# Performance work log

Measured on AMD Instinct MI355X. Metric: run time of the kernel, lower is better.

Reference implementation:

```python
import jax, jax.numpy as jnp
import numpy as np

B = 131072
FLOW_SIZE = 16
PASS = 8
TRANS = FLOW_SIZE - PASS  # 8
N_BINS = 128
HIDDEN = 256


def setup_inputs() -> dict:
    key = jax.random.key(0)
    k0, k1, k2 = jax.random.split(key, 3)
    x = jax.random.uniform(k0, (B, FLOW_SIZE + 1), dtype=jnp.float32)
    W1 = jax.random.normal(k1, (PASS, HIDDEN), dtype=jnp.float32) * 0.3
    b1 = jnp.zeros((HIDDEN,), dtype=jnp.float32)
    W2 = jax.random.normal(k2, (HIDDEN, TRANS * N_BINS), dtype=jnp.float32) * 0.05
    b2 = jnp.zeros((TRANS * N_BINS,), dtype=jnp.float32)
    return {"x": x, "W1": W1, "b1": b1, "W2": W2, "b2": b2}


def reference(x, W1, b1, W2, b2):
    xA = x[:, :PASS]                      # [B, P]
    xB = x[:, PASS:FLOW_SIZE]             # [B, T]
    jacobian = x[:, FLOW_SIZE:FLOW_SIZE + 1]  # [B, 1]

    # NN: small MLP, exp output -> positive unnormalized bin widths Q [B, T, n_bins]
    h = jax.nn.relu(xA @ W1 + b1)
    Q = jnp.exp(h @ W2 + b2).reshape(x.shape[0], TRANS, N_BINS)

    Qsum = jnp.cumsum(Q, axis=-1)                     # [B, T, n_bins]
    Qnorms = Qsum[:, :, -1:]                          # [B, T, 1]
    Q = Q / (Qnorms / N_BINS)                         # normalized slopes
    Qsum = Qsum / Qnorms                              # normalized CDF
    Qsum = jnp.pad(Qsum, ((0, 0), (0, 0), (1, 0)))    # left-pad CDF with 0

    alphas = xB * N_BINS
    bins = jnp.floor(alphas)
    alphas = (alphas - bins) / N_BINS                 # fractional offset within bin
    bins = jnp.clip(bins.astype(jnp.int32), 0, N_BINS - 1)

    cdf_int_part = jnp.take_along_axis(Qsum, bins[..., None], axis=-1)[..., 0]  # [B, T]
    cdf_float_part = jnp.take_along_axis(Q, bins[..., None], axis=-1)[..., 0]   # [B, T]

    cdf = cdf_float_part * alphas + cdf_int_part      # [B, T]
    jacobian = jacobian * jnp.prod(cdf_float_part, axis=-1, keepdims=True)  # [B, 1]

    return jnp.concatenate((xA, cdf, jacobian), axis=-1)  # [B, flow_size+1]
```

## Files before the change

### kernel.cpp

```cpp
#include <hip/hip_runtime.h>
#include <math.h>

#define NROWS 131072
#define XC    17
#define ROWSB 128
#define HID   256
#define NB    128
#define NCOL  1024
#define LOG2E 1.44269504088896340736f

typedef __attribute__((ext_vector_type(8))) short bf16x8;
typedef __attribute__((ext_vector_type(4))) float f32x4;

#if __has_builtin(__builtin_amdgcn_exp2f)
#define EXP2F(v) __builtin_amdgcn_exp2f(v)
#else
#define EXP2F(v) exp2f(v)
#endif
#if __has_builtin(__builtin_amdgcn_rcpf)
#define RCPF(v) __builtin_amdgcn_rcpf(v)
#else
#define RCPF(v) (1.f / (v))
#endif

__device__ __forceinline__ unsigned short f2bf(float f) {
    unsigned int u = __float_as_uint(f);
    return (unsigned short)((u + 0x7FFFu + ((u >> 16) & 1u)) >> 16);
}

__device__ __forceinline__ float red16(float v) {
    int x;
    x = __builtin_amdgcn_update_dpp(0, __float_as_int(v), 0xB1, 0xF, 0xF, true);
    v += __int_as_float(x);
    x = __builtin_amdgcn_update_dpp(0, __float_as_int(v), 0x4E, 0xF, 0xF, true);
    v += __int_as_float(x);
    x = __builtin_amdgcn_update_dpp(0, __float_as_int(v), 0x141, 0xF, 0xF, true);
    v += __int_as_float(x);
    x = __builtin_amdgcn_update_dpp(0, __float_as_int(v), 0x140, 0xF, 0xF, true);
    v += __int_as_float(x);
    return v;
}

__global__ void prep_w2(const float* __restrict__ W2, unsigned short* __restrict__ w2t) {
    __shared__ __align__(16) unsigned short tkT[32][80];
    const int tid = threadIdx.x;
    const int k0 = (blockIdx.x & 3) * 64;
    const int c0 = (blockIdx.x >> 2) * 32;
    const int c4 = (tid & 7) * 4;
    const int kk = (tid >> 3) * 2;
    const float4 r0 = *(const float4*)&W2[(size_t)(k0 + kk) * NCOL + c0 + c4];
    const float4 r1 = *(const float4*)&W2[(size_t)(k0 + kk + 1) * NCOL + c0 + c4];
    const float v0[4] = {r0.x, r0.y, r0.z, r0.w};
    const float v1[4] = {r1.x, r1.y, r1.z, r1.w};
    #pragma unroll
    for (int i = 0; i < 4; ++i) {
        const unsigned int p = (unsigned int)f2bf(v0[i] * LOG2E)
                             | ((unsigned int)f2bf(v1[i] * LOG2E) << 16);
        *(unsigned int*)&tkT[c4 + i][kk] = p;
    }
    __syncthreads();
    const int g = tid & 7, c = tid >> 3;
    const uint4 q = *(const uint4*)&tkT[c][g * 8];
    *(uint4*)&w2t[(size_t)(c0 + c) * HID + k0 + ((g ^ (c & 7)) << 3)] = q;
}

__global__ __launch_bounds__(256, 2)
void gplc6(const float* __restrict__ x,
           const float* __restrict__ W1,
           const float* __restrict__ b1,
           const unsigned short* __restrict__ w2t,
           const float* __restrict__ b2,
           float* __restrict__ out)
{
    __shared__ float xs[ROWSB * XC];
    __shared__ __align__(16) union {
        unsigned short hb[ROWSB * HID];
        struct { unsigned short w2[2][NB * 64]; float b2s[NCOL]; } g;
    } u;

    const int tid  = threadIdx.x;
    const int lane = tid & 63;
    const int w    = tid >> 6;
    const int quad = lane >> 4;
    const int l15  = lane & 15;
    const int wr   = w * 32;
    const int ksw  = (lane & 7) << 3;
    const size_t r0 = (size_t)blockIdx.x * ROWSB;

    for (int i = tid; i < ROWSB * XC; i += 256) xs[i] = x[r0 * XC + i];
    const int cp = tid & 127, hlf = tid >> 7;
    float w1r[16];
    #pragma unroll
    for (int i = 0; i < 8; ++i) {
        const float2 t2 = *(const float2*)&W1[i * HID + 2 * cp];
        w1r[2 * i] = t2.x; w1r[2 * i + 1] = t2.y;
    }
    const float2 b1v = *(const float2*)&b1[2 * cp];
    __syncthreads();

    for (int r = 0; r < 64; ++r) {
        const int row = hlf * 64 + r;
        float a0 = b1v.x, a1 = b1v.y;
        #pragma unroll
        for (int i = 0; i < 8; ++i) {
            const float xv = xs[row * XC + i];
            a0 = fmaf(xv, w1r[2 * i], a0);
            a1 = fmaf(xv, w1r[2 * i + 1], a1);
        }
        a0 = fmaxf(a0, 0.f); a1 = fmaxf(a1, 0.f);
        const int eidx = row * HID + (((cp >> 2) ^ (row & 15)) << 3) + ((cp & 3) << 1);
        *(unsigned int*)&u.hb[eidx] = (unsigned int)f2bf(a0) | ((unsigned int)f2bf(a1) << 16);
    }
    __syncthreads();

    bf16x8 afr[2][8];
    #pragma unroll
    for (int rt = 0; rt < 2; ++rt)
        #pragma unroll
        for (int kf = 0; kf < 8; ++kf) {
            const int row = wr + rt * 16 + l15;
            afr[rt][kf] = *(const bf16x8*)&u.hb[row * HID + (((kf * 4 + quad) ^ l15) << 3)];
        }
    __syncthreads();

    for (int i = tid; i < NCOL; i += 256) u.g.b2s[i] = b2[i] * LOG2E;

    auto stage = [&](int n) {
        const int t = n >> 2, kc = n & 3, buf = n & 1;
        #pragma unroll
        for (int j = 0; j < 4; ++j) {
            const int ob = (w * 4 + j) * 512;
            const int c  = (ob >> 6) + (lane >> 3);
            const int kl = (lane & 7) << 3;
            const unsigned short* gp = w2t + (size_t)(t * NB + c) * HID + kc * 64 + kl;
            unsigned short* lp = &u.g.w2[buf][ob];
            __builtin_amdgcn_global_load_lds(
                (const __attribute__((address_space(1))) unsigned int*)gp,
                (__attribute__((address_space(3))) unsigned int*)lp, 16, 0, 0);
        }
    };

    float jf[2][4] = {{1.f,1.f,1.f,1.f},{1.f,1.f,1.f,1.f}};

    stage(0);
    #pragma unroll 1
    for (int t = 0; t < 8; ++t) {
        f32x4 acc[2][8];
        #pragma unroll
        for (int rt = 0; rt < 2; ++rt)
            #pragma unroll
            for (int ct = 0; ct < 8; ++ct) acc[rt][ct] = (f32x4){0.f, 0.f, 0.f, 0.f};

        #pragma unroll
        for (int kc = 0; kc < 4; ++kc) {
            __syncthreads();
            const int n = t * 4 + kc;
            if (n < 31) stage(n + 1);
            const unsigned short* wsb = u.g.w2[kc & 1];
            #pragma unroll
            for (int ks = 0; ks < 2; ++ks) {
                const int kf = kc * 2 + ks;
                const int klog = ks * 32 + quad * 8;
                #pragma unroll
                for (int ct = 0; ct < 8; ++ct) {
                    const int c = ct * 16 + l15;
                    const bf16x8 bf = *(const bf16x8*)&wsb[c * 64 + (klog ^ ksw)];
                    acc[0][ct] = __builtin_amdgcn_mfma_f32_16x16x32_bf16(afr[0][kf], bf, acc[0][ct], 0, 0, 0);
                    acc[1][ct] = __builtin_amdgcn_mfma_f32_16x16x32_bf16(afr[1][kf], bf, acc[1][ct], 0, 0, 0);
                }
            }
        }

        float bb[8];
        #pragma unroll
        for (int ct = 0; ct < 8; ++ct) bb[ct] = u.g.b2s[t * NB + ct * 16 + l15];
        #pragma unroll
        for (int rt = 0; rt < 2; ++rt)
            #pragma unroll
            for (int i = 0; i < 4; ++i) {
                const int row = wr + rt * 16 + quad * 4 + i;
                const float alpha = xs[row * XC + 8 + t] * 128.f;
                const float fb = floorf(alpha);
                const int bin = min(max((int)fb, 0), 127);
                const float fr = alpha - fb;
                float e[8];
                #pragma unroll
                for (int ct = 0; ct < 8; ++ct) e[ct] = EXP2F(acc[rt][ct][i] + bb[ct]);
                const float P1 = e[0],      P2 = P1 + e[1], P3 = P2 + e[2], P4 = P3 + e[3];
                const float P5 = P4 + e[4], P6 = P5 + e[5], P7 = P6 + e[6], P8 = P7 + e[7];
                int thr = (bin - l15 + 15) >> 4;
                thr = min(max(thr, 0), 8);
                const float sA = (thr & 1) ? P1 : 0.f;
                const float sB = (thr & 1) ? P3 : P2;
                const float sC = (thr & 1) ? P5 : P4;
                const float sD = (thr & 1) ? P7 : P6;
                const float sE = (thr & 2) ? sB : sA;
                const float sF = (thr & 2) ? sD : sC;
                float num = (thr & 4) ? sF : sE;
                num = (thr >= 8) ? P8 : num;
                const int cb = bin >> 4;
                const float t1 = (cb & 1) ? e[1] : e[0];
                const float t2 = (cb & 1) ? e[3] : e[2];
                const float t3 = (cb & 1) ? e[5] : e[4];
                const float t4 = (cb & 1) ? e[7] : e[6];
                const float u1 = (cb & 2) ? t2 : t1;
                const float u2 = (cb & 2) ? t4 : t3;
                const float es = (cb & 4) ? u2 : u1;
                float eb  = ((bin & 15) == l15) ? es : 0.f;
                float tot = P8;
                tot = red16(tot); num = red16(num); eb = red16(eb);
                const float inv = RCPF(tot);
                jf[rt][i] *= 128.f * eb * inv;
                if (l15 == 0) xs[row * XC + 8 + t] = fmaf(eb, fr, num) * inv;
            }
    }

    if (l15 == 0) {
        #pragma unroll
        for (int rt = 0; rt < 2; ++rt)
            #pragma unroll
            for (int i = 0; i < 4; ++i) {
                const int row = wr + rt * 16 + quad * 4 + i;
                xs[row * XC + 16] *= jf[rt][i];
            }
    }
    __syncthreads();
    for (int i = tid; i < ROWSB * XC; i += 256) out[r0 * XC + i] = xs[i];
}

extern "C" void kernel_launch(void* const* d_in, const int* in_sizes, int n_in,
                              void* d_out, int out_size, void* d_ws, size_t ws_size,
                              hipStream_t stream) {
    (void)in_sizes; (void)n_in; (void)ws_size; (void)out_size;
    prep_w2<<<128, 256, 0, stream>>>((const float*)d_in[3], (unsigned short*)d_ws);
    gplc6<<<NROWS / ROWSB, 256, 0, stream>>>(
        (const float*)d_in[0], (const float*)d_in[1], (const float*)d_in[2],
        (const unsigned short*)d_ws, (const float*)d_in[4], (float*)d_out);
}
```

Before: 175.1 us.

## Halve rows per block to raise occupancy and read b2 directly from global

Cuts rows per block from 128 to 64, so each wave handles one 16-row MFMA tile instead of two, and raises launch bounds to 4 blocks per CU. Shared memory and registers per block shrink, and the b2 staging in LDS is dropped in favour of direct global loads added into the accumulators. The aim is more resident waves to hide memory and sync latency. The cost is that every W2 tile is streamed from L2 twice as often per row, with half as much MFMA work per LDS B-fragment load.

```diff
diff --git a/kernel.cpp b/kernel.cpp
--- a/kernel.cpp
+++ b/kernel.cpp
@@ -3,7 +3,7 @@
 
 #define NROWS 131072
 #define XC    17
-#define ROWSB 128
+#define ROWSB 64
 #define HID   256
 #define NB    128
 #define NCOL  1024
@@ -64,7 +64,7 @@
     *(uint4*)&w2t[(size_t)(c0 + c) * HID + k0 + ((g ^ (c & 7)) << 3)] = q;
 }
 
-__global__ __launch_bounds__(256, 2)
+__global__ __launch_bounds__(256, 4)
 void gplc6(const float* __restrict__ x,
            const float* __restrict__ W1,
            const float* __restrict__ b1,
@@ -75,7 +75,7 @@
     __shared__ float xs[ROWSB * XC];
     __shared__ __align__(16) union {
         unsigned short hb[ROWSB * HID];
-        struct { unsigned short w2[2][NB * 64]; float b2s[NCOL]; } g;
+        unsigned short w2[2][NB * 64];
     } u;
 
     const int tid  = threadIdx.x;
@@ -83,7 +83,7 @@
     const int w    = tid >> 6;
     const int quad = lane >> 4;
     const int l15  = lane & 15;
-    const int wr   = w * 32;
+    const int wr   = w * 16;
     const int ksw  = (lane & 7) << 3;
     const size_t r0 = (size_t)blockIdx.x * ROWSB;
 
@@ -98,8 +98,8 @@
     const float2 b1v = *(const float2*)&b1[2 * cp];
     __syncthreads();
 
-    for (int r = 0; r < 64; ++r) {
-        const int row = hlf * 64 + r;
+    for (int r = 0; r < 32; ++r) {
+        const int row = hlf * 32 + r;
         float a0 = b1v.x, a1 = b1v.y;
         #pragma unroll
         for (int i = 0; i < 8; ++i) {
@@ -113,17 +113,13 @@
     }
     __syncthreads();
 
-    bf16x8 afr[2][8];
+    bf16x8 afr[8];
     #pragma unroll
-    for (int rt = 0; rt < 2; ++rt)
-        #pragma unroll
-        for (int kf = 0; kf < 8; ++kf) {
-            const int row = wr + rt * 16 + l15;
-            afr[rt][kf] = *(const bf16x8*)&u.hb[row * HID + (((kf * 4 + quad) ^ l15) << 3)];
-        }
-    __syncthreads();
-
-    for (int i = tid; i < NCOL; i += 256) u.g.b2s[i] = b2[i] * LOG2E;
+    for (int kf = 0; kf < 8; ++kf) {
+        const int row = wr + l15;
+        afr[kf] = *(const bf16x8*)&u.hb[row * HID + (((kf * 4 + quad) ^ l15) << 3)];
+    }
+    __syncthreads();
 
     auto stage = [&](int n) {
         const int t = n >> 2, kc = n & 3, buf = n & 1;
@@ -133,30 +129,28 @@
             const int c  = (ob >> 6) + (lane >> 3);
             const int kl = (lane & 7) << 3;
             const unsigned short* gp = w2t + (size_t)(t * NB + c) * HID + kc * 64 + kl;
-            unsigned short* lp = &u.g.w2[buf][ob];
+            unsigned short* lp = &u.w2[buf][ob];
             __builtin_amdgcn_global_load_lds(
                 (const __attribute__((address_space(1))) unsigned int*)gp,
                 (__attribute__((address_space(3))) unsigned int*)lp, 16, 0, 0);
         }
     };
 
-    float jf[2][4] = {{1.f,1.f,1.f,1.f},{1.f,1.f,1.f,1.f}};
+    float jf[4] = {1.f, 1.f, 1.f, 1.f};
 
     stage(0);
     #pragma unroll 1
     for (int t = 0; t < 8; ++t) {
-        f32x4 acc[2][8];
-        #pragma unroll
-        for (int rt = 0; rt < 2; ++rt)
-            #pragma unroll
-            for (int ct = 0; ct < 8; ++ct) acc[rt][ct] = (f32x4){0.f, 0.f, 0.f, 0.f};
+        f32x4 acc[8];
+        #pragma unroll
+        for (int ct = 0; ct < 8; ++ct) acc[ct] = (f32x4){0.f, 0.f, 0.f, 0.f};
 
         #pragma unroll
         for (int kc = 0; kc < 4; ++kc) {
             __syncthreads();
             const int n = t * 4 + kc;
             if (n < 31) stage(n + 1);
-            const unsigned short* wsb = u.g.w2[kc & 1];
+            const unsigned short* wsb = u.w2[kc & 1];
             #pragma unroll
             for (int ks = 0; ks < 2; ++ks) {
                 const int kf = kc * 2 + ks;
@@ -165,64 +159,62 @@
                 for (int ct = 0; ct < 8; ++ct) {
                     const int c = ct * 16 + l15;
                     const bf16x8 bf = *(const bf16x8*)&wsb[c * 64 + (klog ^ ksw)];
-                    acc[0][ct] = __builtin_amdgcn_mfma_f32_16x16x32_bf16(afr[0][kf], bf, acc[0][ct], 0, 0, 0);
-                    acc[1][ct] = __builtin_amdgcn_mfma_f32_16x16x32_bf16(afr[1][kf], bf, acc[1][ct], 0, 0, 0);
+                    acc[ct] = __builtin_amdgcn_mfma_f32_16x16x32_bf16(afr[kf], bf, acc[ct], 0, 0, 0);
                 }
             }
         }
 
-        float bb[8];
-        #pragma unroll
-        for (int ct = 0; ct < 8; ++ct) bb[ct] = u.g.b2s[t * NB + ct * 16 + l15];
-        #pragma unroll
-        for (int rt = 0; rt < 2; ++rt)
+        #pragma unroll
+        for (int ct = 0; ct < 8; ++ct) {
+            const float bbv = b2[t * NB + ct * 16 + l15] * LOG2E;
+            acc[ct][0] += bbv; acc[ct][1] += bbv; acc[ct][2] += bbv; acc[ct][3] += bbv;
+        }
+
+        #pragma unroll
+        for (int i = 0; i < 4; ++i) {
+            const int row = wr + quad * 4 + i;
+            const float alpha = xs[row * XC + 8 + t] * 128.f;
+            const float fb = floorf(alpha);
+            const int bin = min(max((int)fb, 0), 127);
+            const float fr = alpha - fb;
+            float e[8];
             #pragma unroll
-            for (int i = 0; i < 4; ++i) {
-                const int row = wr + rt * 16 + quad * 4 + i;
-                const float alpha = xs[row * XC + 8 + t] * 128.f;
-                const float fb = floorf(alpha);
-                const int bin = min(max((int)fb, 0), 127);
-                const float fr = alpha - fb;
-                float e[8];
-                #pragma unroll
-                for (int ct = 0; ct < 8; ++ct) e[ct] = EXP2F(acc[rt][ct][i] + bb[ct]);
-                const float P1 = e[0],      P2 = P1 + e[1], P3 = P2 + e[2], P4 = P3 + e[3];
-                const float P5 = P4 + e[4], P6 = P5 + e[5], P7 = P6 + e[6], P8 = P7 + e[7];
-                int thr = (bin - l15 + 15) >> 4;
-                thr = min(max(thr, 0), 8);
-                const float sA = (thr & 1) ? P1 : 0.f;
-                const float sB = (thr & 1) ? P3 : P2;
-                const float sC = (thr & 1) ? P5 : P4;
-                const float sD = (thr & 1) ? P7 : P6;
-                const float sE = (thr & 2) ? sB : sA;
-                const float sF = (thr & 2) ? sD : sC;
-                float num = (thr & 4) ? sF : sE;
-                num = (thr >= 8) ? P8 : num;
-                const int cb = bin >> 4;
-                const float t1 = (cb & 1) ? e[1] : e[0];
-                const float t2 = (cb & 1) ? e[3] : e[2];
-                const float t3 = (cb & 1) ? e[5] : e[4];
-                const float t4 = (cb & 1) ? e[7] : e[6];
-                const float u1 = (cb & 2) ? t2 : t1;
-                const float u2 = (cb & 2) ? t4 : t3;
-                const float es = (cb & 4) ? u2 : u1;
-                float eb  = ((bin & 15) == l15) ? es : 0.f;
-                float tot = P8;
-                tot = red16(tot); num = red16(num); eb = red16(eb);
-                const float inv = RCPF(tot);
-                jf[rt][i] *= 128.f * eb * inv;
-                if (l15 == 0) xs[row * XC + 8 + t] = fmaf(eb, fr, num) * inv;
-            }
+            for (int ct = 0; ct < 8; ++ct) e[ct] = EXP2F(acc[ct][i]);
+            const float P1 = e[0],      P2 = P1 + e[1], P3 = P2 + e[2], P4 = P3 + e[3];
+            const float P5 = P4 + e[4], P6 = P5 + e[5], P7 = P6 + e[6], P8 = P7 + e[7];
+            int thr = (bin - l15 + 15) >> 4;
+            thr = min(max(thr, 0), 8);
+            const float sA = (thr & 1) ? P1 : 0.f;
+            const float sB = (thr & 1) ? P3 : P2;
+            const float sC = (thr & 1) ? P5 : P4;
+            const float sD = (thr & 1) ? P7 : P6;
+            const float sE = (thr & 2) ? sB : sA;
+            const float sF = (thr & 2) ? sD : sC;
+            float num = (thr & 4) ? sF : sE;
+            num = (thr >= 8) ? P8 : num;
+            const int cb = bin >> 4;
+            const float t1 = (cb & 1) ? e[1] : e[0];
+            const float t2 = (cb & 1) ? e[3] : e[2];
+            const float t3 = (cb & 1) ? e[5] : e[4];
+            const float t4 = (cb & 1) ? e[7] : e[6];
+            const float u1 = (cb & 2) ? t2 : t1;
+            const float u2 = (cb & 2) ? t4 : t3;
+            const float es = (cb & 4) ? u2 : u1;
+            float eb  = ((bin & 15) == l15) ? es : 0.f;
+            float tot = P8;
+            tot = red16(tot); num = red16(num); eb = red16(eb);
+            const float inv = RCPF(tot);
+            jf[i] *= 128.f * eb * inv;
+            if (l15 == 0) xs[row * XC + 8 + t] = fmaf(eb, fr, num) * inv;
+        }
     }
 
     if (l15 == 0) {
         #pragma unroll
-        for (int rt = 0; rt < 2; ++rt)
-            #pragma unroll
-            for (int i = 0; i < 4; ++i) {
-                const int row = wr + rt * 16 + quad * 4 + i;
-                xs[row * XC + 16] *= jf[rt][i];
-            }
+        for (int i = 0; i < 4; ++i) {
+            const int row = wr + quad * 4 + i;
+            xs[row * XC + 16] *= jf[i];
+        }
     }
     __syncthreads();
     for (int i = tid; i < ROWSB * XC; i += 256) out[r0 * XC + i] = xs[i];
```

After: 164.0 us. 6.3% less time.

## Halve rows per block and split waves across row and column halves

Applied to the files above, without the earlier changes.

Each block now handles 64 rows instead of 128. Its four waves form a 2x2 grid over row halves and bin-column halves, and the per-row bin sums, CDF numerator and selected bin are merged across the two column waves through a small LDS buffer. The first-layer MLP reads x directly from global, and the b2 bias is read from global per tile instead of being staged in LDS. The launch bound is raised to three blocks per SM. The aim is more resident blocks and smaller register and LDS use per block. The costs are twice as many blocks each streaming the full W2, and an extra barrier plus merge step per transform dimension.

```diff
diff --git a/kernel.cpp b/kernel.cpp
--- a/kernel.cpp
+++ b/kernel.cpp
@@ -3,7 +3,7 @@
 
 #define NROWS 131072
 #define XC    17
-#define ROWSB 128
+#define ROWSB 64
 #define HID   256
 #define NB    128
 #define NCOL  1024
@@ -64,7 +64,7 @@
     *(uint4*)&w2t[(size_t)(c0 + c) * HID + k0 + ((g ^ (c & 7)) << 3)] = q;
 }
 
-__global__ __launch_bounds__(256, 2)
+__global__ __launch_bounds__(256, 3)
 void gplc6(const float* __restrict__ x,
            const float* __restrict__ W1,
            const float* __restrict__ b1,
@@ -75,15 +75,19 @@
     __shared__ float xs[ROWSB * XC];
     __shared__ __align__(16) union {
         unsigned short hb[ROWSB * HID];
-        struct { unsigned short w2[2][NB * 64]; float b2s[NCOL]; } g;
+        struct {
+            unsigned short w2[2][NB * 64];
+            float mrg[2][ROWSB][4];
+        } g;
     } u;
 
     const int tid  = threadIdx.x;
     const int lane = tid & 63;
     const int w    = tid >> 6;
+    const int rw   = w & 1;
+    const int cw   = w >> 1;
     const int quad = lane >> 4;
     const int l15  = lane & 15;
-    const int wr   = w * 32;
     const int ksw  = (lane & 7) << 3;
     const size_t r0 = (size_t)blockIdx.x * ROWSB;
 
@@ -96,14 +100,14 @@
         w1r[2 * i] = t2.x; w1r[2 * i + 1] = t2.y;
     }
     const float2 b1v = *(const float2*)&b1[2 * cp];
-    __syncthreads();
-
-    for (int r = 0; r < 64; ++r) {
-        const int row = hlf * 64 + r;
+
+    for (int r = 0; r < 32; ++r) {
+        const int row = __builtin_amdgcn_readfirstlane(hlf * 32 + r);
+        const float* xr = x + (r0 + row) * XC;
         float a0 = b1v.x, a1 = b1v.y;
         #pragma unroll
         for (int i = 0; i < 8; ++i) {
-            const float xv = xs[row * XC + i];
+            const float xv = xr[i];
             a0 = fmaf(xv, w1r[2 * i], a0);
             a1 = fmaf(xv, w1r[2 * i + 1], a1);
         }
@@ -118,12 +122,10 @@
     for (int rt = 0; rt < 2; ++rt)
         #pragma unroll
         for (int kf = 0; kf < 8; ++kf) {
-            const int row = wr + rt * 16 + l15;
+            const int row = rw * 32 + rt * 16 + l15;
             afr[rt][kf] = *(const bf16x8*)&u.hb[row * HID + (((kf * 4 + quad) ^ l15) << 3)];
         }
     __syncthreads();
-
-    for (int i = tid; i < NCOL; i += 256) u.g.b2s[i] = b2[i] * LOG2E;
 
     auto stage = [&](int n) {
         const int t = n >> 2, kc = n & 3, buf = n & 1;
@@ -145,11 +147,11 @@
     stage(0);
     #pragma unroll 1
     for (int t = 0; t < 8; ++t) {
-        f32x4 acc[2][8];
+        f32x4 acc[2][4];
         #pragma unroll
         for (int rt = 0; rt < 2; ++rt)
             #pragma unroll
-            for (int ct = 0; ct < 8; ++ct) acc[rt][ct] = (f32x4){0.f, 0.f, 0.f, 0.f};
+            for (int ct = 0; ct < 4; ++ct) acc[rt][ct] = (f32x4){0.f, 0.f, 0.f, 0.f};
 
         #pragma unroll
         for (int kc = 0; kc < 4; ++kc) {
@@ -162,8 +164,8 @@
                 const int kf = kc * 2 + ks;
                 const int klog = ks * 32 + quad * 8;
                 #pragma unroll
-                for (int ct = 0; ct < 8; ++ct) {
-                    const int c = ct * 16 + l15;
+                for (int ct = 0; ct < 4; ++ct) {
+                    const int c = cw * 64 + ct * 16 + l15;
                     const bf16x8 bf = *(const bf16x8*)&wsb[c * 64 + (klog ^ ksw)];
                     acc[0][ct] = __builtin_amdgcn_mfma_f32_16x16x32_bf16(afr[0][kf], bf, acc[0][ct], 0, 0, 0);
                     acc[1][ct] = __builtin_amdgcn_mfma_f32_16x16x32_bf16(afr[1][kf], bf, acc[1][ct], 0, 0, 0);
@@ -171,56 +173,72 @@
             }
         }
 
-        float bb[8];
-        #pragma unroll
-        for (int ct = 0; ct < 8; ++ct) bb[ct] = u.g.b2s[t * NB + ct * 16 + l15];
+        float bb[4];
+        #pragma unroll
+        for (int ct = 0; ct < 4; ++ct)
+            bb[ct] = b2[t * NB + cw * 64 + ct * 16 + l15] * LOG2E;
+
         #pragma unroll
         for (int rt = 0; rt < 2; ++rt)
             #pragma unroll
             for (int i = 0; i < 4; ++i) {
-                const int row = wr + rt * 16 + quad * 4 + i;
+                const int row = rw * 32 + rt * 16 + quad * 4 + i;
                 const float alpha = xs[row * XC + 8 + t] * 128.f;
                 const float fb = floorf(alpha);
                 const int bin = min(max((int)fb, 0), 127);
-                const float fr = alpha - fb;
-                float e[8];
+                float e[4];
                 #pragma unroll
-                for (int ct = 0; ct < 8; ++ct) e[ct] = EXP2F(acc[rt][ct][i] + bb[ct]);
-                const float P1 = e[0],      P2 = P1 + e[1], P3 = P2 + e[2], P4 = P3 + e[3];
-                const float P5 = P4 + e[4], P6 = P5 + e[5], P7 = P6 + e[6], P8 = P7 + e[7];
-                int thr = (bin - l15 + 15) >> 4;
-                thr = min(max(thr, 0), 8);
+                for (int ct = 0; ct < 4; ++ct) e[ct] = EXP2F(acc[rt][ct][i] + bb[ct]);
+                const float P1 = e[0], P2 = P1 + e[1], P3 = P2 + e[2], P4 = P3 + e[3];
+                const int bl = bin - cw * 64;
+                int thr = (bl - l15 + 15) >> 4;
+                thr = min(max(thr, 0), 4);
                 const float sA = (thr & 1) ? P1 : 0.f;
                 const float sB = (thr & 1) ? P3 : P2;
-                const float sC = (thr & 1) ? P5 : P4;
-                const float sD = (thr & 1) ? P7 : P6;
-                const float sE = (thr & 2) ? sB : sA;
-                const float sF = (thr & 2) ? sD : sC;
-                float num = (thr & 4) ? sF : sE;
-                num = (thr >= 8) ? P8 : num;
-                const int cb = bin >> 4;
-                const float t1 = (cb & 1) ? e[1] : e[0];
-                const float t2 = (cb & 1) ? e[3] : e[2];
-                const float t3 = (cb & 1) ? e[5] : e[4];
-                const float t4 = (cb & 1) ? e[7] : e[6];
-                const float u1 = (cb & 2) ? t2 : t1;
-                const float u2 = (cb & 2) ? t4 : t3;
-                const float es = (cb & 4) ? u2 : u1;
-                float eb  = ((bin & 15) == l15) ? es : 0.f;
-                float tot = P8;
+                float num = (thr & 2) ? sB : sA;
+                num = (thr >= 4) ? P4 : num;
+                const int cbl = bl >> 4;
+                const float t1 = (cbl & 1) ? e[1] : e[0];
+                const float t2 = (cbl & 1) ? e[3] : e[2];
+                const float es = (cbl & 2) ? t2 : t1;
+                float eb = (((unsigned)bl < 64u) && ((bin & 15) == l15)) ? es : 0.f;
+                float tot = P4;
                 tot = red16(tot); num = red16(num); eb = red16(eb);
-                const float inv = RCPF(tot);
-                jf[rt][i] *= 128.f * eb * inv;
-                if (l15 == 0) xs[row * XC + 8 + t] = fmaf(eb, fr, num) * inv;
+                if (l15 == 0) {
+                    const f32x4 tr = {tot, num, eb, 0.f};
+                    *(f32x4*)&u.g.mrg[cw][row][0] = tr;
+                }
             }
-    }
-
-    if (l15 == 0) {
+        __syncthreads();
+
+        if (cw == 0) {
+            #pragma unroll
+            for (int rt = 0; rt < 2; ++rt)
+                #pragma unroll
+                for (int i = 0; i < 4; ++i) {
+                    const int row = rw * 32 + rt * 16 + quad * 4 + i;
+                    if (l15 == 0) {
+                        const f32x4 pa = *(const f32x4*)&u.g.mrg[0][row][0];
+                        const f32x4 pb = *(const f32x4*)&u.g.mrg[1][row][0];
+                        const float T   = pa[0] + pb[0];
+                        const float nm  = pa[1] + pb[1];
+                        const float ebv = pa[2] + pb[2];
+                        const float alpha = xs[row * XC + 8 + t] * 128.f;
+                        const float fr = alpha - floorf(alpha);
+                        const float inv = RCPF(T);
+                        jf[rt][i] *= 128.f * ebv * inv;
+                        xs[row * XC + 8 + t] = fmaf(ebv, fr, nm) * inv;
+                    }
+                }
+        }
+    }
+
+    if (cw == 0 && l15 == 0) {
         #pragma unroll
         for (int rt = 0; rt < 2; ++rt)
             #pragma unroll
             for (int i = 0; i < 4; ++i) {
-                const int row = wr + rt * 16 + quad * 4 + i;
+                const int row = rw * 32 + rt * 16 + quad * 4 + i;
                 xs[row * XC + 16] *= jf[rt][i];
             }
     }
```

New measurement: 205.8 us. 1.18x slower.

## Load W2 MFMA fragments directly from global into registers, dropping LDS staging

Applied to the files above, without the earlier changes.

The prep kernel now lays W2 out in MFMA B-fragment order, so each lane loads its bf16x8 operands with coalesced 16-byte global loads straight into registers. These loads are double-buffered across k-slices. This removes the LDS double-buffer, the async global-to-LDS copies, and the per-stage __syncthreads barriers from the GEMM loop. MFMA bursts are wrapped in s_setprio, and b2 is read directly from global. In exchange, every wave re-reads W2 from L2/global instead of sharing one LDS copy per block, and register pressure rises from the two 8-fragment buffers.

```diff
diff --git a/kernel.cpp b/kernel.cpp
--- a/kernel.cpp
+++ b/kernel.cpp
@@ -41,42 +41,35 @@
     return v;
 }
 
-__global__ void prep_w2(const float* __restrict__ W2, unsigned short* __restrict__ w2t) {
-    __shared__ __align__(16) unsigned short tkT[32][80];
-    const int tid = threadIdx.x;
-    const int k0 = (blockIdx.x & 3) * 64;
-    const int c0 = (blockIdx.x >> 2) * 32;
-    const int c4 = (tid & 7) * 4;
-    const int kk = (tid >> 3) * 2;
-    const float4 r0 = *(const float4*)&W2[(size_t)(k0 + kk) * NCOL + c0 + c4];
-    const float4 r1 = *(const float4*)&W2[(size_t)(k0 + kk + 1) * NCOL + c0 + c4];
-    const float v0[4] = {r0.x, r0.y, r0.z, r0.w};
-    const float v1[4] = {r1.x, r1.y, r1.z, r1.w};
+__global__ void prep_w2f(const float* __restrict__ W2, unsigned short* __restrict__ w2f) {
+    const int tid  = threadIdx.x;
+    const int F    = blockIdx.x * 4 + (tid >> 6);
+    const int lane = tid & 63;
+    const int quad = lane >> 4, l15 = lane & 15;
+    const int ct = F & 7, ks = (F >> 3) & 1, kc = (F >> 4) & 3, t = F >> 6;
+    const int k0  = kc * 64 + ks * 32 + quad * 8;
+    const int col = t * NB + ct * 16 + l15;
+    unsigned int p[4];
     #pragma unroll
-    for (int i = 0; i < 4; ++i) {
-        const unsigned int p = (unsigned int)f2bf(v0[i] * LOG2E)
-                             | ((unsigned int)f2bf(v1[i] * LOG2E) << 16);
-        *(unsigned int*)&tkT[c4 + i][kk] = p;
-    }
-    __syncthreads();
-    const int g = tid & 7, c = tid >> 3;
-    const uint4 q = *(const uint4*)&tkT[c][g * 8];
-    *(uint4*)&w2t[(size_t)(c0 + c) * HID + k0 + ((g ^ (c & 7)) << 3)] = q;
+    for (int jj = 0; jj < 4; ++jj) {
+        const unsigned short lo = f2bf(W2[(size_t)(k0 + 2 * jj)     * NCOL + col] * LOG2E);
+        const unsigned short hi = f2bf(W2[(size_t)(k0 + 2 * jj + 1) * NCOL + col] * LOG2E);
+        p[jj] = (unsigned int)lo | ((unsigned int)hi << 16);
+    }
+    uint4 q; q.x = p[0]; q.y = p[1]; q.z = p[2]; q.w = p[3];
+    *(uint4*)&w2f[(size_t)F * 512 + lane * 8] = q;
 }
 
 __global__ __launch_bounds__(256, 2)
 void gplc6(const float* __restrict__ x,
            const float* __restrict__ W1,
            const float* __restrict__ b1,
-           const unsigned short* __restrict__ w2t,
+           const unsigned short* __restrict__ w2f,
            const float* __restrict__ b2,
            float* __restrict__ out)
 {
     __shared__ float xs[ROWSB * XC];
-    __shared__ __align__(16) union {
-        unsigned short hb[ROWSB * HID];
-        struct { unsigned short w2[2][NB * 64]; float b2s[NCOL]; } g;
-    } u;
+    __shared__ __align__(16) unsigned short hb[ROWSB * HID];
 
     const int tid  = threadIdx.x;
     const int lane = tid & 63;
@@ -84,7 +77,6 @@
     const int quad = lane >> 4;
     const int l15  = lane & 15;
     const int wr   = w * 32;
-    const int ksw  = (lane & 7) << 3;
     const size_t r0 = (size_t)blockIdx.x * ROWSB;
 
     for (int i = tid; i < ROWSB * XC; i += 256) xs[i] = x[r0 * XC + i];
@@ -109,7 +101,7 @@
         }
         a0 = fmaxf(a0, 0.f); a1 = fmaxf(a1, 0.f);
         const int eidx = row * HID + (((cp >> 2) ^ (row & 15)) << 3) + ((cp & 3) << 1);
-        *(unsigned int*)&u.hb[eidx] = (unsigned int)f2bf(a0) | ((unsigned int)f2bf(a1) << 16);
+        *(unsigned int*)&hb[eidx] = (unsigned int)f2bf(a0) | ((unsigned int)f2bf(a1) << 16);
     }
     __syncthreads();
 
@@ -119,30 +111,34 @@
         #pragma unroll
         for (int kf = 0; kf < 8; ++kf) {
             const int row = wr + rt * 16 + l15;
-            afr[rt][kf] = *(const bf16x8*)&u.hb[row * HID + (((kf * 4 + quad) ^ l15) << 3)];
+            afr[rt][kf] = *(const bf16x8*)&hb[row * HID + (((kf * 4 + quad) ^ l15) << 3)];
         }
-    __syncthreads();
-
-    for (int i = tid; i < NCOL; i += 256) u.g.b2s[i] = b2[i] * LOG2E;
-
-    auto stage = [&](int n) {
-        const int t = n >> 2, kc = n & 3, buf = n & 1;
-        #pragma unroll
-        for (int j = 0; j < 4; ++j) {
-            const int ob = (w * 4 + j) * 512;
-            const int c  = (ob >> 6) + (lane >> 3);
-            const int kl = (lane & 7) << 3;
-            const unsigned short* gp = w2t + (size_t)(t * NB + c) * HID + kc * 64 + kl;
-            unsigned short* lp = &u.g.w2[buf][ob];
-            __builtin_amdgcn_global_load_lds(
-                (const __attribute__((address_space(1))) unsigned int*)gp,
-                (__attribute__((address_space(3))) unsigned int*)lp, 16, 0, 0);
-        }
+
+    const int loff = lane * 8;
+    auto loadslice = [&](bf16x8* d, int g) {
+        const unsigned short* fp = w2f + (size_t)g * 4096 + loff;
+        #pragma unroll
+        for (int ct = 0; ct < 8; ++ct)
+            d[ct] = *(const bf16x8*)&fp[ct * 512];
     };
 
     float jf[2][4] = {{1.f,1.f,1.f,1.f},{1.f,1.f,1.f,1.f}};
-
-    stage(0);
+    bf16x8 bA[8], bB[8];
+
+#define SLICE_MFMA(CUR, KF)                                                     \
+    {                                                                           \
+        __builtin_amdgcn_s_setprio(1);                                          \
+        _Pragma("unroll")                                                       \
+        for (int ct = 0; ct < 8; ++ct) {                                        \
+            acc[0][ct] = __builtin_amdgcn_mfma_f32_16x16x32_bf16(               \
+                afr[0][KF], CUR[ct], acc[0][ct], 0, 0, 0);                      \
+            acc[1][ct] = __builtin_amdgcn_mfma_f32_16x16x32_bf16(               \
+                afr[1][KF], CUR[ct], acc[1][ct], 0, 0, 0);                      \
+        }                                                                       \
+        __builtin_amdgcn_s_setprio(0);                                          \
+    }
+
+    loadslice(bA, 0);
     #pragma unroll 1
     for (int t = 0; t < 8; ++t) {
         f32x4 acc[2][8];
@@ -151,29 +147,25 @@
             #pragma unroll
             for (int ct = 0; ct < 8; ++ct) acc[rt][ct] = (f32x4){0.f, 0.f, 0.f, 0.f};
 
-        #pragma unroll
-        for (int kc = 0; kc < 4; ++kc) {
-            __syncthreads();
-            const int n = t * 4 + kc;
-            if (n < 31) stage(n + 1);
-            const unsigned short* wsb = u.g.w2[kc & 1];
-            #pragma unroll
-            for (int ks = 0; ks < 2; ++ks) {
-                const int kf = kc * 2 + ks;
-                const int klog = ks * 32 + quad * 8;
-                #pragma unroll
-                for (int ct = 0; ct < 8; ++ct) {
-                    const int c = ct * 16 + l15;
-                    const bf16x8 bf = *(const bf16x8*)&wsb[c * 64 + (klog ^ ksw)];
-                    acc[0][ct] = __builtin_amdgcn_mfma_f32_16x16x32_bf16(afr[0][kf], bf, acc[0][ct], 0, 0, 0);
-                    acc[1][ct] = __builtin_amdgcn_mfma_f32_16x16x32_bf16(afr[1][kf], bf, acc[1][ct], 0, 0, 0);
-                }
+        float bb[8];
+        #pragma unroll
+        for (int ct = 0; ct < 8; ++ct) bb[ct] = b2[t * NB + ct * 16 + l15] * LOG2E;
+
+        const int g0 = t * 8;
+        #pragma unroll
+        for (int sp = 0; sp < 4; ++sp) {
+            {
+                const int g = g0 + 2 * sp;
+                if (g < 63) loadslice(bB, g + 1);
+                SLICE_MFMA(bA, 2 * sp)
+            }
+            {
+                const int g = g0 + 2 * sp + 1;
+                if (g < 63) loadslice(bA, g + 1);
+                SLICE_MFMA(bB, 2 * sp + 1)
             }
         }
 
-        float bb[8];
-        #pragma unroll
-        for (int ct = 0; ct < 8; ++ct) bb[ct] = u.g.b2s[t * NB + ct * 16 + l15];
         #pragma unroll
         for (int rt = 0; rt < 2; ++rt)
             #pragma unroll
@@ -214,6 +206,7 @@
                 if (l15 == 0) xs[row * XC + 8 + t] = fmaf(eb, fr, num) * inv;
             }
     }
+#undef SLICE_MFMA
 
     if (l15 == 0) {
         #pragma unroll
@@ -232,7 +225,7 @@
                               void* d_out, int out_size, void* d_ws, size_t ws_size,
                               hipStream_t stream) {
     (void)in_sizes; (void)n_in; (void)ws_size; (void)out_size;
-    prep_w2<<<128, 256, 0, stream>>>((const float*)d_in[3], (unsigned short*)d_ws);
+    prep_w2f<<<128, 256, 0, stream>>>((const float*)d_in[3], (unsigned short*)d_ws);
     gplc6<<<NROWS / ROWSB, 256, 0, stream>>>(
         (const float*)d_in[0], (const float*)d_in[1], (const float*)d_in[2],
         (const unsigned short*)d_ws, (const float*)d_in[4], (float*)d_out);
```

After: 167.0 us. 4.6% less time.
